# Optimization experiments

Measured on AMD Instinct MI355X. Metric: run time of the kernel, lower is better.

## Reference

```python
import jax, jax.numpy as jnp
import numpy as np

WIN_H, WIN_W = 4, 7
WIN = WIN_H * WIN_W  # 28 sample points == feature channels
GRID_OFF = (0.0, 40.0)
SPATIAL_SCALE = 1.0 / 0.4
BN_EPS = 1e-3


def setup_inputs() -> dict:
    key = jax.random.key(0)
    ks = jax.random.split(key, 5)
    B, Cin, H, W = 4, 256, 200, 176
    Cout, N = WIN, 2048
    x = jax.random.normal(ks[0], (B, Cin, H, W), dtype=jnp.float32)
    # boxes [x, y, z, w, l, h, r] in realistic KITTI ranges
    lo = jnp.array([0.0, -40.0, -3.0, 1.5, 3.2, 1.4, -np.pi], jnp.float32)
    hi = jnp.array([70.0, 40.0, 1.0, 2.0, 4.2, 1.8, np.pi], jnp.float32)
    u = jax.random.uniform(ks[1], (B, N, 7), dtype=jnp.float32)
    guided_anchors = lo + u * (hi - lo)
    w1 = jax.random.normal(ks[2], (Cout, Cin, 3, 3), jnp.float32) * 0.02
    gamma = jnp.ones((Cout,), jnp.float32)
    beta = jnp.zeros((Cout,), jnp.float32)
    running_mean = jnp.zeros((Cout,), jnp.float32)
    running_var = jnp.ones((Cout,), jnp.float32)
    w2 = jax.random.normal(ks[3], (Cout, Cout, 1, 1), jnp.float32) * 0.05
    return dict(x=x, guided_anchors=guided_anchors, w1=w1, gamma=gamma,
                beta=beta, running_mean=running_mean, running_var=running_var, w2=w2)


def _convs(x, w1, gamma, beta, mean, var, w2):
    dn = ('NCHW', 'OIHW', 'NCHW')
    y = jax.lax.conv_general_dilated(x, w1, (1, 1), 'SAME', dimension_numbers=dn)
    scale = gamma * jax.lax.rsqrt(var + BN_EPS)
    y = y * scale[:, None, None] + (beta - mean * scale)[:, None, None]  # BN (inference)
    y = jax.nn.relu(y)
    return jax.lax.conv_general_dilated(y, w2, (1, 1), 'SAME', dimension_numbers=dn)


def _gen_sample_grid(box5):
    xg, yg, wg, lg, rg = (box5[:, i] for i in range(5))
    c = jnp.cos(rg)[:, None, None]
    s = jnp.sin(rg)[:, None, None]
    xx = (jnp.linspace(-0.5, 0.5, WIN_H)[None, :] * wg[:, None])[:, :, None]  # (N,4,1)
    yy = (jnp.linspace(-0.5, 0.5, WIN_W)[None, :] * lg[:, None])[:, None, :]  # (N,1,7)
    xpix = xx * c + yy * s + xg[:, None, None]  # (N,4,7)
    ypix = yy * c - xx * s + yg[:, None, None]  # (N,4,7)
    xs = ((jnp.transpose(xpix, (1, 2, 0)) + GRID_OFF[0]) * SPATIAL_SCALE).reshape(WIN, -1)
    ys = ((jnp.transpose(ypix, (1, 2, 0)) + GRID_OFF[1]) * SPATIAL_SCALE).reshape(WIN, -1)
    return xs, ys


def _bilinear_sample(img, xs, ys):
    # img: (C,H,W); xs, ys: (C,N) pixel coords (align_corners=True semantics,
    # zero padding outside) -> (C,N). Channel c samples at grid row c.
    C, H, W = img.shape
    x0 = jnp.floor(xs); y0 = jnp.floor(ys)
    wx = xs - x0; wy = ys - y0
    cidx = jnp.arange(C)[:, None]

    def gather(yf, xf):
        yi = yf.astype(jnp.int32); xi = xf.astype(jnp.int32)
        valid = (yf >= 0) & (yf <= H - 1) & (xf >= 0) & (xf <= W - 1)
        v = img[cidx, jnp.clip(yi, 0, H - 1), jnp.clip(xi, 0, W - 1)]
        return jnp.where(valid, v, 0.0)

    return (gather(y0, x0) * (1 - wx) * (1 - wy)
            + gather(y0, x0 + 1) * wx * (1 - wy)
            + gather(y0 + 1, x0) * (1 - wx) * wy
            + gather(y0 + 1, x0 + 1) * wx * wy)


def reference(x, guided_anchors, w1, gamma, beta, running_mean, running_var, w2):
    feat = _convs(x, w1, gamma, beta, running_mean, running_var, w2)  # (B,28,H,W)
    box5 = guided_anchors[:, :, jnp.array([0, 1, 3, 4, 6])]           # (B,N,5)
    xs, ys = jax.vmap(_gen_sample_grid)(box5)                          # (B,28,N) each
    vals = jax.vmap(_bilinear_sample)(feat, xs, ys)                    # (B,28,N)
    scores = jnp.mean(vals, axis=1)                                    # (B,N)
    return scores.reshape(-1)                                          # (B*N,)
```

## Files before the change

### kernel.cpp

```cpp
#include <hip/hip_runtime.h>
#include <hip/hip_bf16.h>

#define HH 200
#define WW 176
#define CIN 256
#define CO 28
#define BN_EPS 1e-3f

typedef __attribute__((ext_vector_type(8))) short short8;
typedef __attribute__((ext_vector_type(4))) float f32x4;

static __device__ __forceinline__ ushort f2bf(float f) {
    __hip_bfloat16 h = __float2bfloat16(f);
    return __builtin_bit_cast(ushort, h);
}

__global__ void prep_k(const float* __restrict__ w1, const float* __restrict__ gamma,
                       const float* __restrict__ beta, const float* __restrict__ mean,
                       const float* __restrict__ var, ushort* __restrict__ w1b,
                       float* __restrict__ shift)
{
    int idx = blockIdx.x * 256 + threadIdx.x;
    if (idx < CO) {
        float sc = gamma[idx] * rsqrtf(var[idx] + BN_EPS);
        shift[idx] = beta[idx] - mean[idx] * sc;
    }
    if (idx < 8 * 9 * 2 * 64 * 8) {
        int j   = idx & 7;
        int l   = (idx >> 3) & 63;
        int n   = (idx >> 9) & 1;
        int rem = idx >> 10;
        int t   = rem % 9;
        int h   = rem / 9;
        int co = n * 16 + (l & 15);
        int ci = h * 32 + (l >> 4) * 8 + j;
        float v = 0.f;
        if (co < CO) {
            float sc = gamma[co] * rsqrtf(var[co] + BN_EPS);
            v = w1[(co * CIN + ci) * 9 + t] * sc;
        }
        w1b[idx] = f2bf(v);
    }
}

__global__ __launch_bounds__(256, 3) void conv_mfma_k(
    const float* __restrict__ x, const ushort* __restrict__ w1b,
    const float* __restrict__ shift, float* __restrict__ y1)
{
    __shared__ uint4 sbuf[2][192 * 4];

    const int tid  = threadIdx.x;
    const int lane = tid & 63;
    const int w    = tid >> 6;
    const int wu   = __builtin_amdgcn_readfirstlane(w);
    const int c_   = lane & 15;
    const int oct  = lane >> 4;

    const int NB = 11 * 25 * 4;
    const int q = NB / 8, r = NB % 8;
    const int bid  = blockIdx.x;
    const int xcd  = bid & 7;
    const int rank = bid >> 3;
    const int tile = (xcd < r ? xcd * (q + 1) : r * (q + 1) + (xcd - r) * q) + rank;

    const int tx  = tile % 11;
    const int rem = tile / 11;
    const int ty  = rem % 25;
    const int b   = rem / 25;
    const int x0  = tx * 16, y0 = ty * 8;

    const float* xb = x + (size_t)b * CIN * HH * WW;

    int  soff[3]; bool sval[3];
#pragma unroll
    for (int it = 0; it < 3; ++it) {
        int p = it * 64 + lane;
        int rr = p / 18, cc = p - rr * 18;
        int gy = y0 + rr - 1, gx = x0 + cc - 1;
        bool v = (gy >= 0) & (gy < HH) & (gx >= 0) & (gx < WW);
        sval[it] = v;
        soff[it] = v ? gy * WW + gx : 0;
    }
    const uint voff0 = (uint)(soff[0] * 4);
    const uint voff1 = (uint)(soff[1] * 4);
    const uint voff2 = (uint)(soff[2] * 4);
    const uint wvoff = (uint)(lane * 16);

    float  xr[24];
    short8 wr[18];

    f32x4 acc[2][2];
#pragma unroll
    for (int m = 0; m < 2; ++m)
#pragma unroll
        for (int n = 0; n < 2; ++n)
            acc[m][n] = (f32x4){0.f, 0.f, 0.f, 0.f};

#define XLOAD(h)                                                              \
    {                                                                         \
        _Pragma("unroll")                                                     \
        for (int j = 0; j < 8; ++j) {                                         \
            const float* bj = xb + (size_t)((h) * 32 + wu * 8 + j) * 35200;   \
            asm volatile("global_load_dword %0, %1, %2"                       \
                         : "=v"(xr[0 + j]) : "v"(voff0), "s"(bj));            \
            asm volatile("global_load_dword %0, %1, %2"                       \
                         : "=v"(xr[8 + j]) : "v"(voff1), "s"(bj));            \
            asm volatile("global_load_dword %0, %1, %2"                       \
                         : "=v"(xr[16 + j]) : "v"(voff2), "s"(bj));           \
        }                                                                     \
    }

#define WLOAD(h)                                                              \
    {                                                                         \
        _Pragma("unroll")                                                     \
        for (int k = 0; k < 18; ++k) {                                        \
            const ushort* bk = w1b + (size_t)(h) * 9216 + k * 512;            \
            asm volatile("global_load_dwordx4 %0, %1, %2"                     \
                         : "=v"(wr[k]) : "v"(wvoff), "s"(bk));                \
        }                                                                     \
    }

#define WAITW(N)                                                              \
    asm volatile("s_waitcnt vmcnt(" #N ")"                                    \
        : "+v"(wr[0]), "+v"(wr[1]), "+v"(wr[2]), "+v"(wr[3]), "+v"(wr[4]),    \
          "+v"(wr[5]), "+v"(wr[6]), "+v"(wr[7]), "+v"(wr[8]));                \
    asm volatile("s_waitcnt vmcnt(" #N ")"                                    \
        : "+v"(wr[9]), "+v"(wr[10]), "+v"(wr[11]), "+v"(wr[12]),              \
          "+v"(wr[13]), "+v"(wr[14]), "+v"(wr[15]), "+v"(wr[16]),             \
          "+v"(wr[17]));                                                      \
    __builtin_amdgcn_sched_barrier(0);

#define WAITX()                                                               \
    asm volatile("s_waitcnt vmcnt(0)"                                         \
        : "+v"(xr[0]), "+v"(xr[1]), "+v"(xr[2]), "+v"(xr[3]), "+v"(xr[4]),    \
          "+v"(xr[5]), "+v"(xr[6]), "+v"(xr[7]), "+v"(xr[8]), "+v"(xr[9]),    \
          "+v"(xr[10]), "+v"(xr[11]));                                        \
    asm volatile("s_waitcnt vmcnt(0)"                                         \
        : "+v"(xr[12]), "+v"(xr[13]), "+v"(xr[14]), "+v"(xr[15]),             \
          "+v"(xr[16]), "+v"(xr[17]), "+v"(xr[18]), "+v"(xr[19]),             \
          "+v"(xr[20]), "+v"(xr[21]), "+v"(xr[22]), "+v"(xr[23]));            \
    __builtin_amdgcn_sched_barrier(0);

#define PACK_WR(BI)                                                           \
    {                                                                         \
        _Pragma("unroll")                                                     \
        for (int it = 0; it < 3; ++it) {                                      \
            int p = it * 64 + lane;                                           \
            ushort u[8];                                                      \
            _Pragma("unroll")                                                 \
            for (int j = 0; j < 8; ++j)                                       \
                u[j] = sval[it] ? f2bf(xr[it * 8 + j]) : (ushort)0;           \
            uint4 val;                                                        \
            val.x = (uint)u[0] | ((uint)u[1] << 16);                          \
            val.y = (uint)u[2] | ((uint)u[3] << 16);                          \
            val.z = (uint)u[4] | ((uint)u[5] << 16);                          \
            val.w = (uint)u[6] | ((uint)u[7] << 16);                          \
            sbuf[BI][p * 4 + ((w + (p >> 1)) & 3)] = val;                     \
        }                                                                     \
    }

#define COMPUTE(h)                                                            \
    {                                                                         \
        const uint4* sb = sbuf[(h) & 1];                                      \
        _Pragma("unroll")                                                     \
        for (int dx = 0; dx < 3; ++dx) {                                      \
            short8 av[4];                                                     \
            _Pragma("unroll")                                                 \
            for (int rl = 0; rl < 4; ++rl) {                                  \
                int p = (2 * w + rl) * 18 + c_ + dx;                          \
                av[rl] = __builtin_bit_cast(short8,                           \
                    sb[p * 4 + ((oct + (p >> 1)) & 3)]);                      \
            }                                                                 \
            _Pragma("unroll")                                                 \
            for (int dy = 0; dy < 3; ++dy) {                                  \
                const int t = dy * 3 + dx;                                    \
                _Pragma("unroll")                                             \
                for (int m = 0; m < 2; ++m) {                                 \
                    acc[m][0] = __builtin_amdgcn_mfma_f32_16x16x32_bf16(      \
                        av[m + dy], wr[t * 2 + 0], acc[m][0], 0, 0, 0);       \
                    acc[m][1] = __builtin_amdgcn_mfma_f32_16x16x32_bf16(      \
                        av[m + dy], wr[t * 2 + 1], acc[m][1], 0, 0, 0);       \
                }                                                             \
            }                                                                 \
        }                                                                     \
    }

#define BODY(h)                                                               \
    {                                                                         \
        XLOAD((h) + 1);                                                       \
        WAITW(24)                                                             \
        COMPUTE(h);                                                           \
        WAITX()                                                               \
        PACK_WR(((h) + 1) & 1);                                               \
        WLOAD((h) + 1);                                                       \
        asm volatile("s_waitcnt lgkmcnt(0)");                                 \
        __builtin_amdgcn_sched_barrier(0);                                    \
        __builtin_amdgcn_s_barrier();                                         \
    }

    WLOAD(0);
    XLOAD(0);
    WAITW(0)
    WAITX()
    PACK_WR(0);
    asm volatile("s_waitcnt lgkmcnt(0)");
    __builtin_amdgcn_sched_barrier(0);
    __builtin_amdgcn_s_barrier();

    BODY(0) BODY(1) BODY(2) BODY(3) BODY(4) BODY(5) BODY(6)
    WAITW(0)
    COMPUTE(7);

    const int co0 = c_;
    const int co1 = 16 + c_;
    const float s0 = shift[co0];
    const float s1 = (co1 < CO) ? shift[co1] : 0.f;
#pragma unroll
    for (int m = 0; m < 2; ++m) {
        int gy = y0 + 2 * w + m;
#pragma unroll
        for (int reg = 0; reg < 4; ++reg) {
            int gx = x0 + oct * 4 + reg;
            float* yp = y1 + ((size_t)(b * HH + gy) * WW + gx) * CO;
            float v0 = acc[m][0][reg] + s0;
            yp[co0] = v0 > 0.f ? v0 : 0.f;
            if (co1 < CO) {
                float v1 = acc[m][1][reg] + s1;
                yp[co1] = v1 > 0.f ? v1 : 0.f;
            }
        }
    }
}

__global__ __launch_bounds__(224) void sample_k(
    const float* __restrict__ y1, const float* __restrict__ ga,
    const float* __restrict__ w2, float* __restrict__ out)
{
    __shared__ float red[224];
    const int lb  = threadIdx.x / CO;
    const int k   = threadIdx.x % CO;
    const int box = blockIdx.x * 8 + lb;
    const int b   = box >> 11;

    const float* ap = ga + (size_t)box * 7;
    float xg = ap[0], yg = ap[1], wg = ap[3], lg = ap[4], rg = ap[6];
    float c = cosf(rg), s = sinf(rg);

    const int i = k / 7, j = k % 7;
    float xx = ((float)i * (1.f / 3.f) - 0.5f) * wg;
    float yy = ((float)j * (1.f / 6.f) - 0.5f) * lg;
    float xs = (xx * c + yy * s + xg) * 2.5f;
    float ys = (yy * c - xx * s + yg + 40.f) * 2.5f;

    float x0 = floorf(xs), y0 = floorf(ys);
    float wx = xs - x0,    wy = ys - y0;

    float w2r[CO];
    const float* w2p = w2 + k * CO;
#pragma unroll
    for (int q = 0; q < 7; ++q) {
        float4 t = ((const float4*)w2p)[q];
        w2r[4*q] = t.x; w2r[4*q+1] = t.y; w2r[4*q+2] = t.z; w2r[4*q+3] = t.w;
    }

    float val = 0.f;
    const float* yb = y1 + (size_t)b * HH * WW * CO;
#pragma unroll
    for (int cor = 0; cor < 4; ++cor) {
        float yf = y0 + (float)(cor >> 1);
        float xf = x0 + (float)(cor & 1);
        float cw = ((cor & 1) ? wx : 1.f - wx) * ((cor >> 1) ? wy : 1.f - wy);
        if (yf >= 0.f && yf <= (float)(HH - 1) && xf >= 0.f && xf <= (float)(WW - 1)) {
            int yi = (int)yf, xi = (int)xf;
            const float* p = yb + ((size_t)yi * WW + xi) * CO;
            float d = 0.f;
#pragma unroll
            for (int q = 0; q < 7; ++q) {
                float4 t = ((const float4*)p)[q];
                d = fmaf(w2r[4*q],   t.x, d);
                d = fmaf(w2r[4*q+1], t.y, d);
                d = fmaf(w2r[4*q+2], t.z, d);
                d = fmaf(w2r[4*q+3], t.w, d);
            }
            val = fmaf(cw, d, val);
        }
    }

    red[threadIdx.x] = val;
    __syncthreads();
    if (k == 0) {
        float sum = 0.f;
#pragma unroll
        for (int q = 0; q < CO; ++q) sum += red[lb * CO + q];
        out[box] = sum * (1.f / 28.f);
    }
}

extern "C" void kernel_launch(void* const* d_in, const int* in_sizes, int n_in,
                              void* d_out, int out_size, void* d_ws, size_t ws_size,
                              hipStream_t stream) {
    const float* x     = (const float*)d_in[0];
    const float* ga    = (const float*)d_in[1];
    const float* w1    = (const float*)d_in[2];
    const float* gamma = (const float*)d_in[3];
    const float* beta  = (const float*)d_in[4];
    const float* mean  = (const float*)d_in[5];
    const float* var   = (const float*)d_in[6];
    const float* w2    = (const float*)d_in[7];
    float* out = (float*)d_out;

    ushort* w1b   = (ushort*)d_ws;
    float*  shift = (float*)((char*)d_ws + 147456);
    float*  y1    = (float*)((char*)d_ws + 147968);

    prep_k<<<(8 * 9 * 2 * 64 * 8 + 255) / 256, 256, 0, stream>>>(
        w1, gamma, beta, mean, var, w1b, shift);

    conv_mfma_k<<<11 * 25 * 4, 256, 0, stream>>>(x, w1b, shift, y1);

    sample_k<<<(4 * 2048) / 8, 224, 0, stream>>>(y1, ga, w2, out);
}
```

Measured before the change: 83.46 us.

## Split conv input channels across waves with private LDS and cross-wave reduction

The 3x3 conv kernel moves from a row split, where each wave computes two output rows over all input channels with block-wide double buffering and barriers per chunk, to a channel split. Each wave now owns two 32-channel chunks, stages its own LDS slice, computes all eight output rows, and the four partial accumulators are summed through LDS at the end. The goal is to drop per-chunk block barriers and give each wave more independent MFMA work. In exchange, register pressure rises (16 accumulators, launch bounds lowered to 2 blocks per SIMD), a final reduction pass is added, and there is less overlap between loads and compute inside a wave.

```diff
diff --git a/kernel.cpp b/kernel.cpp
--- a/kernel.cpp
+++ b/kernel.cpp
@@ -43,11 +43,11 @@
     }
 }
 
-__global__ __launch_bounds__(256, 3) void conv_mfma_k(
+__global__ __launch_bounds__(256, 2) void conv_mfma_k(
     const float* __restrict__ x, const ushort* __restrict__ w1b,
     const float* __restrict__ shift, float* __restrict__ y1)
 {
-    __shared__ uint4 sbuf[2][192 * 4];
+    __shared__ uint4 sbuf[4][768];
 
     const int tid  = threadIdx.x;
     const int lane = tid & 63;
@@ -86,62 +86,42 @@
     const uint voff2 = (uint)(soff[2] * 4);
     const uint wvoff = (uint)(lane * 16);
 
-    float  xr[24];
-    short8 wr[18];
-
-    f32x4 acc[2][2];
-#pragma unroll
-    for (int m = 0; m < 2; ++m)
+    float  xA[24], xB[24];
+    short8 wqA[6], wqB[6];
+
+    f32x4 acc[8][2];
+#pragma unroll
+    for (int m = 0; m < 8; ++m)
 #pragma unroll
         for (int n = 0; n < 2; ++n)
             acc[m][n] = (f32x4){0.f, 0.f, 0.f, 0.f};
 
-#define XLOAD(h)                                                              \
+#define ISSUE24(ch, o, XR)                                                    \
     {                                                                         \
         _Pragma("unroll")                                                     \
         for (int j = 0; j < 8; ++j) {                                         \
-            const float* bj = xb + (size_t)((h) * 32 + wu * 8 + j) * 35200;   \
+            const float* bj = xb + (size_t)((ch) * 32 + (o) * 8 + j) * 35200; \
             asm volatile("global_load_dword %0, %1, %2"                       \
-                         : "=v"(xr[0 + j]) : "v"(voff0), "s"(bj));            \
+                         : "=v"(XR[0 + j]) : "v"(voff0), "s"(bj));            \
             asm volatile("global_load_dword %0, %1, %2"                       \
-                         : "=v"(xr[8 + j]) : "v"(voff1), "s"(bj));            \
+                         : "=v"(XR[8 + j]) : "v"(voff1), "s"(bj));            \
             asm volatile("global_load_dword %0, %1, %2"                       \
-                         : "=v"(xr[16 + j]) : "v"(voff2), "s"(bj));           \
-        }                                                                     \
-    }
-
-#define WLOAD(h)                                                              \
-    {                                                                         \
-        _Pragma("unroll")                                                     \
-        for (int k = 0; k < 18; ++k) {                                        \
-            const ushort* bk = w1b + (size_t)(h) * 9216 + k * 512;            \
-            asm volatile("global_load_dwordx4 %0, %1, %2"                     \
-                         : "=v"(wr[k]) : "v"(wvoff), "s"(bk));                \
-        }                                                                     \
-    }
-
-#define WAITW(N)                                                              \
+                         : "=v"(XR[16 + j]) : "v"(voff2), "s"(bj));           \
+        }                                                                     \
+    }
+
+#define WAITX(N, XR)                                                          \
     asm volatile("s_waitcnt vmcnt(" #N ")"                                    \
-        : "+v"(wr[0]), "+v"(wr[1]), "+v"(wr[2]), "+v"(wr[3]), "+v"(wr[4]),    \
-          "+v"(wr[5]), "+v"(wr[6]), "+v"(wr[7]), "+v"(wr[8]));                \
+        : "+v"(XR[0]), "+v"(XR[1]), "+v"(XR[2]), "+v"(XR[3]), "+v"(XR[4]),    \
+          "+v"(XR[5]), "+v"(XR[6]), "+v"(XR[7]), "+v"(XR[8]), "+v"(XR[9]),    \
+          "+v"(XR[10]), "+v"(XR[11]));                                        \
     asm volatile("s_waitcnt vmcnt(" #N ")"                                    \
-        : "+v"(wr[9]), "+v"(wr[10]), "+v"(wr[11]), "+v"(wr[12]),              \
-          "+v"(wr[13]), "+v"(wr[14]), "+v"(wr[15]), "+v"(wr[16]),             \
-          "+v"(wr[17]));                                                      \
+        : "+v"(XR[12]), "+v"(XR[13]), "+v"(XR[14]), "+v"(XR[15]),             \
+          "+v"(XR[16]), "+v"(XR[17]), "+v"(XR[18]), "+v"(XR[19]),             \
+          "+v"(XR[20]), "+v"(XR[21]), "+v"(XR[22]), "+v"(XR[23]));            \
     __builtin_amdgcn_sched_barrier(0);
 
-#define WAITX()                                                               \
-    asm volatile("s_waitcnt vmcnt(0)"                                         \
-        : "+v"(xr[0]), "+v"(xr[1]), "+v"(xr[2]), "+v"(xr[3]), "+v"(xr[4]),    \
-          "+v"(xr[5]), "+v"(xr[6]), "+v"(xr[7]), "+v"(xr[8]), "+v"(xr[9]),    \
-          "+v"(xr[10]), "+v"(xr[11]));                                        \
-    asm volatile("s_waitcnt vmcnt(0)"                                         \
-        : "+v"(xr[12]), "+v"(xr[13]), "+v"(xr[14]), "+v"(xr[15]),             \
-          "+v"(xr[16]), "+v"(xr[17]), "+v"(xr[18]), "+v"(xr[19]),             \
-          "+v"(xr[20]), "+v"(xr[21]), "+v"(xr[22]), "+v"(xr[23]));            \
-    __builtin_amdgcn_sched_barrier(0);
-
-#define PACK_WR(BI)                                                           \
+#define PACK(XR, o)                                                           \
     {                                                                         \
         _Pragma("unroll")                                                     \
         for (int it = 0; it < 3; ++it) {                                      \
@@ -149,84 +129,117 @@
             ushort u[8];                                                      \
             _Pragma("unroll")                                                 \
             for (int j = 0; j < 8; ++j)                                       \
-                u[j] = sval[it] ? f2bf(xr[it * 8 + j]) : (ushort)0;           \
+                u[j] = sval[it] ? f2bf(XR[it * 8 + j]) : (ushort)0;           \
             uint4 val;                                                        \
             val.x = (uint)u[0] | ((uint)u[1] << 16);                          \
             val.y = (uint)u[2] | ((uint)u[3] << 16);                          \
             val.z = (uint)u[4] | ((uint)u[5] << 16);                          \
             val.w = (uint)u[6] | ((uint)u[7] << 16);                          \
-            sbuf[BI][p * 4 + ((w + (p >> 1)) & 3)] = val;                     \
-        }                                                                     \
-    }
-
-#define COMPUTE(h)                                                            \
-    {                                                                         \
-        const uint4* sb = sbuf[(h) & 1];                                      \
-        _Pragma("unroll")                                                     \
-        for (int dx = 0; dx < 3; ++dx) {                                      \
-            short8 av[4];                                                     \
+            sbuf[w][p * 4 + (((o) + (p >> 1)) & 3)] = val;                    \
+        }                                                                     \
+    }
+
+#define WLOAD6(ch, dx, WQ)                                                    \
+    {                                                                         \
+        const ushort* wbase = w1b + (size_t)(ch) * 9216;                      \
+        _Pragma("unroll")                                                     \
+        for (int dy = 0; dy < 3; ++dy) {                                      \
             _Pragma("unroll")                                                 \
-            for (int rl = 0; rl < 4; ++rl) {                                  \
-                int p = (2 * w + rl) * 18 + c_ + dx;                          \
-                av[rl] = __builtin_bit_cast(short8,                           \
-                    sb[p * 4 + ((oct + (p >> 1)) & 3)]);                      \
+            for (int n = 0; n < 2; ++n) {                                     \
+                const ushort* bk = wbase + (size_t)((dy * 3 + (dx)) * 2 + n) * 512; \
+                asm volatile("global_load_dwordx4 %0, %1, %2"                 \
+                             : "=v"(WQ[dy * 2 + n]) : "v"(wvoff), "s"(bk));   \
             }                                                                 \
+        }                                                                     \
+    }
+
+#define WAITW(N, WQ)                                                          \
+    asm volatile("s_waitcnt vmcnt(" #N ")"                                    \
+        : "+v"(WQ[0]), "+v"(WQ[1]), "+v"(WQ[2]), "+v"(WQ[3]), "+v"(WQ[4]),    \
+          "+v"(WQ[5]));                                                       \
+    __builtin_amdgcn_sched_barrier(0);
+
+#define COMP_DX(dx, WQ)                                                       \
+    {                                                                         \
+        short8 av[10];                                                        \
+        _Pragma("unroll")                                                     \
+        for (int rr = 0; rr < 10; ++rr) {                                     \
+            int p = rr * 18 + c_ + (dx);                                      \
+            av[rr] = __builtin_bit_cast(short8,                               \
+                sbuf[w][p * 4 + ((oct + (p >> 1)) & 3)]);                     \
+        }                                                                     \
+        _Pragma("unroll")                                                     \
+        for (int dy = 0; dy < 3; ++dy) {                                      \
             _Pragma("unroll")                                                 \
-            for (int dy = 0; dy < 3; ++dy) {                                  \
-                const int t = dy * 3 + dx;                                    \
-                _Pragma("unroll")                                             \
-                for (int m = 0; m < 2; ++m) {                                 \
-                    acc[m][0] = __builtin_amdgcn_mfma_f32_16x16x32_bf16(      \
-                        av[m + dy], wr[t * 2 + 0], acc[m][0], 0, 0, 0);       \
-                    acc[m][1] = __builtin_amdgcn_mfma_f32_16x16x32_bf16(      \
-                        av[m + dy], wr[t * 2 + 1], acc[m][1], 0, 0, 0);       \
-                }                                                             \
+            for (int m = 0; m < 8; ++m) {                                     \
+                acc[m][0] = __builtin_amdgcn_mfma_f32_16x16x32_bf16(          \
+                    av[m + dy], WQ[dy * 2 + 0], acc[m][0], 0, 0, 0);          \
+                acc[m][1] = __builtin_amdgcn_mfma_f32_16x16x32_bf16(          \
+                    av[m + dy], WQ[dy * 2 + 1], acc[m][1], 0, 0, 0);          \
             }                                                                 \
         }                                                                     \
     }
 
-#define BODY(h)                                                               \
-    {                                                                         \
-        XLOAD((h) + 1);                                                       \
-        WAITW(24)                                                             \
-        COMPUTE(h);                                                           \
-        WAITX()                                                               \
-        PACK_WR(((h) + 1) & 1);                                               \
-        WLOAD((h) + 1);                                                       \
-        asm volatile("s_waitcnt lgkmcnt(0)");                                 \
-        __builtin_amdgcn_sched_barrier(0);                                    \
-        __builtin_amdgcn_s_barrier();                                         \
-    }
-
-    WLOAD(0);
-    XLOAD(0);
-    WAITW(0)
-    WAITX()
-    PACK_WR(0);
-    asm volatile("s_waitcnt lgkmcnt(0)");
-    __builtin_amdgcn_sched_barrier(0);
-    __builtin_amdgcn_s_barrier();
-
-    BODY(0) BODY(1) BODY(2) BODY(3) BODY(4) BODY(5) BODY(6)
-    WAITW(0)
-    COMPUTE(7);
-
-    const int co0 = c_;
-    const int co1 = 16 + c_;
-    const float s0 = shift[co0];
-    const float s1 = (co1 < CO) ? shift[co1] : 0.f;
-#pragma unroll
-    for (int m = 0; m < 2; ++m) {
-        int gy = y0 + 2 * w + m;
-#pragma unroll
-        for (int reg = 0; reg < 4; ++reg) {
-            int gx = x0 + oct * 4 + reg;
-            float* yp = y1 + ((size_t)(b * HH + gy) * WW + gx) * CO;
-            float v0 = acc[m][0][reg] + s0;
-            yp[co0] = v0 > 0.f ? v0 : 0.f;
-            if (co1 < CO) {
-                float v1 = acc[m][1][reg] + s1;
-                yp[co1] = v1 > 0.f ? v1 : 0.f;
+#define STAGE(ch)                                                             \
+    {                                                                         \
+        ISSUE24(ch, 0, xA); ISSUE24(ch, 1, xB);                               \
+        WAITX(24, xA) PACK(xA, 0);                                            \
+        ISSUE24(ch, 2, xA);                                                   \
+        WAITX(24, xB) PACK(xB, 1);                                            \
+        ISSUE24(ch, 3, xB);                                                   \
+        WAITX(24, xA) PACK(xA, 2);                                            \
+        WLOAD6(ch, 0, wqA);                                                   \
+        WAITX(6, xB) PACK(xB, 3);                                             \
+    }
+
+#define COMPCH(ch)                                                            \
+    {                                                                         \
+        WLOAD6(ch, 1, wqB);                                                   \
+        WAITW(6, wqA) COMP_DX(0, wqA);                                        \
+        WLOAD6(ch, 2, wqA);                                                   \
+        WAITW(6, wqB) COMP_DX(1, wqB);                                        \
+        WAITW(0, wqA) COMP_DX(2, wqA);                                        \
+    }
+
+    STAGE(wu)
+    COMPCH(wu)
+    STAGE(wu + 4)
+    COMPCH(wu + 4)
+
+    __syncthreads();
+    f32x4* rb = (f32x4*)&sbuf[0][0];
+    if (w > 0) {
+        int base = (w - 1) * 1024 + lane;
+#pragma unroll
+        for (int m = 0; m < 8; ++m)
+#pragma unroll
+            for (int n = 0; n < 2; ++n)
+                rb[base + (m * 2 + n) * 64] = acc[m][n];
+    }
+    __syncthreads();
+    if (w == 0) {
+        const float s0 = shift[c_];
+        const float s1 = (16 + c_ < CO) ? shift[16 + c_] : 0.f;
+#pragma unroll
+        for (int m = 0; m < 8; ++m) {
+            int gy = y0 + m;
+#pragma unroll
+            for (int n = 0; n < 2; ++n) {
+                f32x4 s = acc[m][n];
+#pragma unroll
+                for (int v = 1; v < 4; ++v)
+                    s += rb[(v - 1) * 1024 + (m * 2 + n) * 64 + lane];
+                const float sh = n ? s1 : s0;
+                const int co = n * 16 + c_;
+                if (co < CO) {
+#pragma unroll
+                    for (int reg = 0; reg < 4; ++reg) {
+                        int gx = x0 + oct * 4 + reg;
+                        float* yp = y1 + ((size_t)(b * HH + gy) * WW + gx) * CO;
+                        float vv = s[reg] + sh;
+                        yp[co] = vv > 0.f ? vv : 0.f;
+                    }
+                }
             }
         }
     }
```

Measured after the change: 75.51 us. 1.11x faster.
